# Performance work log

Hardware: AMD Instinct MI355X
Metric: run time of the kernel (lower is better)

The kernel has to match this reference:

```python
import jax, jax.numpy as jnp
import numpy as np

TOP_K = 2
SCALING = 32.0 / 16.0  # alpha / rank


def setup_inputs() -> dict:
    key = jax.random.key(0)
    ks = jax.random.split(key, 8)
    B_, S, D = 4, 4096, 2048
    E, R, H = 5, 16, 256
    return {
        "x": jax.random.normal(ks[0], (B_, S, D), jnp.float32),
        "base_output": jax.random.normal(ks[1], (B_, S, D), jnp.float32),
        "A": jax.random.normal(ks[2], (E, D, R), jnp.float32) * (1.0 / R),
        "B": jax.random.normal(ks[3], (E, R, D), jnp.float32) * 0.02,
        "W1": jax.random.normal(ks[4], (D, H), jnp.float32) * (1.0 / np.sqrt(D)),
        "b1": jnp.zeros((H,), jnp.float32),
        "W2": jax.random.normal(ks[5], (H, E), jnp.float32) * (1.0 / np.sqrt(H)),
        "b2": jnp.zeros((E,), jnp.float32),
    }


def reference(x, base_output, A, B, W1, b1, W2, b2):
    # Router: Linear -> SiLU -> Linear -> softmax
    routing_logits = jax.nn.silu(x @ W1 + b1) @ W2 + b2          # [B,S,E]
    routing_weights = jax.nn.softmax(routing_logits, axis=-1)
    top_k_weights, top_k_indices = jax.lax.top_k(routing_weights, TOP_K)  # [B,S,K]
    top_k_weights = top_k_weights / top_k_weights.sum(-1, keepdims=True)

    # Dense per-expert LoRA eval (faithful to original): x @ A_e @ B_e * scaling
    low = jnp.einsum('bsd,edr->bser', x, A)                       # [B,S,E,R]
    expert_outputs = jnp.einsum('bser,erd->bsed', low, B) * SCALING  # [B,S,E,D]

    # Gather selected experts and combine with normalized weights
    gathered = jnp.take_along_axis(expert_outputs, top_k_indices[..., None], axis=2)  # [B,S,K,D]
    combined = (gathered * top_k_weights[..., None]).sum(axis=2)  # [B,S,D]
    return base_output + combined
```

## Files before the change

kernel.cpp:

```cpp
#include <hip/hip_runtime.h>
#include <math.h>

#define N_TOK 16384
#define D_DIM 2048
#define H_DIM 256
#define E_NUM 5
#define R_DIM 16
#define ER 80

#define NCT 21
#define KG_N 64

typedef _Float16 half8 __attribute__((ext_vector_type(8)));
typedef float f32x4 __attribute__((ext_vector_type(4)));

__global__ __launch_bounds__(256) void pack_w_kernel(
    const float* __restrict__ W1, const float* __restrict__ A,
    _Float16* __restrict__ Whi, _Float16* __restrict__ Wlo) {
  const int idx = blockIdx.x * 256 + threadIdx.x;
  const int lane = idx & 63;
  const int kgct = idx >> 6;
  const int kg = kgct & 63;
  const int ct = kgct >> 6;
  const int k0 = kg * 32 + ((lane >> 4) << 3);
  const int par = lane & 15;
  float v[8];
  if (ct < 16) {
    const int col = ct * 16 + par;
#pragma unroll
    for (int j = 0; j < 8; ++j) v[j] = W1[(size_t)(k0 + j) * H_DIM + col];
  } else {
    const float* Ae = A + (size_t)(ct - 16) * D_DIM * R_DIM;
#pragma unroll
    for (int j = 0; j < 8; ++j) v[j] = Ae[(size_t)(k0 + j) * R_DIM + par];
  }
  half8 hv, lv;
#pragma unroll
  for (int j = 0; j < 8; ++j) {
    const _Float16 hh = (_Float16)v[j];
    hv[j] = hh;
    lv[j] = (_Float16)(v[j] - (float)hh);
  }
  ((half8*)Whi)[(size_t)kgct * 64 + lane] = hv;
  ((half8*)Wlo)[(size_t)kgct * 64 + lane] = lv;
}

__global__ __launch_bounds__(256, 3) void xgemm_kernel(
    const float* __restrict__ x, const float* __restrict__ b1,
    const _Float16* __restrict__ Whi, const _Float16* __restrict__ Wlo,
    float* __restrict__ h, float* __restrict__ P) {
  __shared__ _Float16 lds[2][2][4][64][8];
  const int t = threadIdx.x;
  const int tok0 = blockIdx.x * 64;
  const int y = blockIdx.y;
  const int lane = t & 63;
  const int w = t >> 6;
  const int sr = t >> 2;
  const int sq = t & 3;
  const int lq = lane >> 4;
  const int lp = lane & 15;

  const float* xrow = x + (size_t)(tok0 + sr) * D_DIM + (sq << 3);

  {
    float xv[8];
    *(float4*)&xv[0] = *(const float4*)(xrow);
    *(float4*)&xv[4] = *(const float4*)(xrow + 4);
    half8 hv, lv;
#pragma unroll
    for (int j = 0; j < 8; ++j) {
      const _Float16 hh = (_Float16)xv[j];
      hv[j] = hh;
      lv[j] = (_Float16)(xv[j] - (float)hh);
    }
    *(half8*)&lds[0][0][sq][sr][0] = hv;
    *(half8*)&lds[0][1][sq][sr][0] = lv;
  }

  const half8* WH = (const half8*)Whi;
  const half8* WL = (const half8*)Wlo;

  if (y < 2) {
    f32x4 acc[4][2];
#pragma unroll
    for (int i = 0; i < 4; ++i)
#pragma unroll
      for (int j = 0; j < 2; ++j) acc[i][j] = (f32x4)0.f;
    const int ctg0 = (y << 3) + (w << 1);
    int cur = 0;
    for (int kg = 0; kg < KG_N; ++kg) {
      __syncthreads();
      float xv[8];
      if (kg < KG_N - 1) {
        *(float4*)&xv[0] = *(const float4*)(xrow + (kg + 1) * 32);
        *(float4*)&xv[4] = *(const float4*)(xrow + (kg + 1) * 32 + 4);
      }
      half8 bh[2], bl[2], ah[4], al[4];
#pragma unroll
      for (int ct = 0; ct < 2; ++ct) {
        const size_t wo = ((size_t)(ctg0 + ct) * 64 + kg) * 64 + lane;
        bh[ct] = WH[wo];
        bl[ct] = WL[wo];
      }
#pragma unroll
      for (int rt = 0; rt < 4; ++rt) {
        ah[rt] = *(const half8*)&lds[cur][0][lq][(rt << 4) + lp][0];
        al[rt] = *(const half8*)&lds[cur][1][lq][(rt << 4) + lp][0];
      }
#pragma unroll
      for (int rt = 0; rt < 4; ++rt)
#pragma unroll
        for (int ct = 0; ct < 2; ++ct) {
          acc[rt][ct] = __builtin_amdgcn_mfma_f32_16x16x32_f16(al[rt], bh[ct], acc[rt][ct], 0, 0, 0);
          acc[rt][ct] = __builtin_amdgcn_mfma_f32_16x16x32_f16(ah[rt], bl[ct], acc[rt][ct], 0, 0, 0);
          acc[rt][ct] = __builtin_amdgcn_mfma_f32_16x16x32_f16(ah[rt], bh[ct], acc[rt][ct], 0, 0, 0);
        }
      if (kg < KG_N - 1) {
        half8 hv, lv;
#pragma unroll
        for (int j = 0; j < 8; ++j) {
          const _Float16 hh = (_Float16)xv[j];
          hv[j] = hh;
          lv[j] = (_Float16)(xv[j] - (float)hh);
        }
        *(half8*)&lds[cur ^ 1][0][sq][sr][0] = hv;
        *(half8*)&lds[cur ^ 1][1][sq][sr][0] = lv;
      }
      cur ^= 1;
    }
    const int colb = (y << 7) + (w << 5);
#pragma unroll
    for (int rt = 0; rt < 4; ++rt)
#pragma unroll
      for (int ct = 0; ct < 2; ++ct) {
        const int col = colb + (ct << 4) + lp;
        const float bb = b1[col];
#pragma unroll
        for (int rg = 0; rg < 4; ++rg) {
          const int row = tok0 + (rt << 4) + (lq << 2) + rg;
          float v = acc[rt][ct][rg] + bb;
          v = v / (1.f + expf(-v));
          h[(size_t)row * H_DIM + col] = v;
        }
      }
  } else {
    f32x4 acc[5];
#pragma unroll
    for (int j = 0; j < 5; ++j) acc[j] = (f32x4)0.f;
    int cur = 0;
    for (int kg = 0; kg < KG_N; ++kg) {
      __syncthreads();
      float xv[8];
      if (kg < KG_N - 1) {
        *(float4*)&xv[0] = *(const float4*)(xrow + (kg + 1) * 32);
        *(float4*)&xv[4] = *(const float4*)(xrow + (kg + 1) * 32 + 4);
      }
      half8 bh[5], bl[5];
#pragma unroll
      for (int ct = 0; ct < 5; ++ct) {
        const size_t wo = ((size_t)(16 + ct) * 64 + kg) * 64 + lane;
        bh[ct] = WH[wo];
        bl[ct] = WL[wo];
      }
      const half8 ah = *(const half8*)&lds[cur][0][lq][(w << 4) + lp][0];
      const half8 al = *(const half8*)&lds[cur][1][lq][(w << 4) + lp][0];
#pragma unroll
      for (int ct = 0; ct < 5; ++ct) {
        acc[ct] = __builtin_amdgcn_mfma_f32_16x16x32_f16(al, bh[ct], acc[ct], 0, 0, 0);
        acc[ct] = __builtin_amdgcn_mfma_f32_16x16x32_f16(ah, bl[ct], acc[ct], 0, 0, 0);
        acc[ct] = __builtin_amdgcn_mfma_f32_16x16x32_f16(ah, bh[ct], acc[ct], 0, 0, 0);
      }
      if (kg < KG_N - 1) {
        half8 hv, lv;
#pragma unroll
        for (int j = 0; j < 8; ++j) {
          const _Float16 hh = (_Float16)xv[j];
          hv[j] = hh;
          lv[j] = (_Float16)(xv[j] - (float)hh);
        }
        *(half8*)&lds[cur ^ 1][0][sq][sr][0] = hv;
        *(half8*)&lds[cur ^ 1][1][sq][sr][0] = lv;
      }
      cur ^= 1;
    }
#pragma unroll
    for (int ct = 0; ct < 5; ++ct)
#pragma unroll
      for (int rg = 0; rg < 4; ++rg) {
        const int row = tok0 + (w << 4) + (lq << 2) + rg;
        P[(size_t)row * ER + (ct << 4) + lp] = acc[ct][rg];
      }
  }
}

__global__ __launch_bounds__(256) void route_kernel(
    const float* __restrict__ h, const float* __restrict__ W2,
    const float* __restrict__ b2, float* __restrict__ P) {
  __shared__ float w2s[H_DIM * E_NUM];
  const int t = threadIdx.x;
  for (int i = t; i < H_DIM * E_NUM; i += 256) w2s[i] = W2[i];
  __syncthreads();

  const int tok = blockIdx.x * 64 + (t >> 2);
  const int part = t & 3;
  float p[5] = {0.f, 0.f, 0.f, 0.f, 0.f};
  const float* hr = h + (size_t)tok * H_DIM + part * 64;
#pragma unroll
  for (int i = 0; i < 16; ++i) {
    float hv[4];
    *(float4*)hv = *(const float4*)(hr + (i << 2));
#pragma unroll
    for (int u = 0; u < 4; ++u) {
      const int c = part * 64 + (i << 2) + u;
#pragma unroll
      for (int e = 0; e < 5; ++e) p[e] = fmaf(hv[u], w2s[c * 5 + e], p[e]);
    }
  }
#pragma unroll
  for (int e = 0; e < 5; ++e) {
    p[e] += __shfl_xor(p[e], 1, 64);
    p[e] += __shfl_xor(p[e], 2, 64);
    p[e] += b2[e];
  }
  int e0 = 0;
#pragma unroll
  for (int e = 1; e < 5; ++e) if (p[e] > p[e0]) e0 = e;
  int e1 = (e0 == 0) ? 1 : 0;
#pragma unroll
  for (int e = 0; e < 5; ++e) if (e != e0 && p[e] > p[e1]) e1 = e;
  const float q = expf(p[e1] - p[e0]);
  const float s0 = 2.f / (1.f + q);
  const float s1 = q * s0;

  float* pr = P + (size_t)tok * ER + part * 20;
#pragma unroll
  for (int g = 0; g < 5; ++g) {
    float pv[4];
    *(float4*)pv = *(const float4*)(pr + (g << 2));
#pragma unroll
    for (int u = 0; u < 4; ++u) {
      const int e = (part * 20 + (g << 2) + u) >> 4;
      const float s = (e == e0) ? s0 : ((e == e1) ? s1 : 0.f);
      pv[u] *= s;
    }
    *(float4*)(pr + (g << 2)) = *(float4*)pv;
  }
}

__global__ __launch_bounds__(256) void combine_kernel(
    const float* __restrict__ P, const float* __restrict__ Bm,
    const float* __restrict__ base, float* __restrict__ out) {
  const int t = threadIdx.x;
  const int wg = __builtin_amdgcn_readfirstlane(t >> 6);
  const int c4 = ((blockIdx.x & 7) << 8) + ((t & 63) << 2);
  const int tok0 = ((blockIdx.x >> 3) << 6) + (wg << 4);

  float4 acc[16];
#pragma unroll
  for (int i = 0; i < 16; ++i) acc[i] = make_float4(0.f, 0.f, 0.f, 0.f);

  for (int k0 = 0; k0 < ER; k0 += 4) {
    const float4 bv0 = *(const float4*)(Bm + (size_t)(k0 + 0) * D_DIM + c4);
    const float4 bv1 = *(const float4*)(Bm + (size_t)(k0 + 1) * D_DIM + c4);
    const float4 bv2 = *(const float4*)(Bm + (size_t)(k0 + 2) * D_DIM + c4);
    const float4 bv3 = *(const float4*)(Bm + (size_t)(k0 + 3) * D_DIM + c4);
#pragma unroll
    for (int i = 0; i < 16; ++i) {
      const float* pr = P + (size_t)(tok0 + i) * ER + k0;
      const float p0 = pr[0], p1 = pr[1], p2 = pr[2], p3 = pr[3];
      acc[i].x = fmaf(p0, bv0.x, fmaf(p1, bv1.x, fmaf(p2, bv2.x, fmaf(p3, bv3.x, acc[i].x))));
      acc[i].y = fmaf(p0, bv0.y, fmaf(p1, bv1.y, fmaf(p2, bv2.y, fmaf(p3, bv3.y, acc[i].y))));
      acc[i].z = fmaf(p0, bv0.z, fmaf(p1, bv1.z, fmaf(p2, bv2.z, fmaf(p3, bv3.z, acc[i].z))));
      acc[i].w = fmaf(p0, bv0.w, fmaf(p1, bv1.w, fmaf(p2, bv2.w, fmaf(p3, bv3.w, acc[i].w))));
    }
  }

#pragma unroll
  for (int i = 0; i < 16; ++i) {
    const size_t o = (size_t)(tok0 + i) * D_DIM + c4;
    const float4 b = *(const float4*)(base + o);
    float4 r;
    r.x = acc[i].x + b.x;
    r.y = acc[i].y + b.y;
    r.z = acc[i].z + b.z;
    r.w = acc[i].w + b.w;
    *(float4*)(out + o) = r;
  }
}

extern "C" void kernel_launch(void* const* d_in, const int* in_sizes, int n_in,
                              void* d_out, int out_size, void* d_ws,
                              size_t ws_size, hipStream_t stream) {
  const float* x  = (const float*)d_in[0];
  const float* bo = (const float*)d_in[1];
  const float* A  = (const float*)d_in[2];
  const float* Bm = (const float*)d_in[3];
  const float* W1 = (const float*)d_in[4];
  const float* b1 = (const float*)d_in[5];
  const float* W2 = (const float*)d_in[6];
  const float* b2 = (const float*)d_in[7];
  float* out = (float*)d_out;

  char* ws = (char*)d_ws;
  float* h = (float*)ws;
  float* P = (float*)(ws + 16777216);
  _Float16* Whi = (_Float16*)(ws + 16777216 + 5242880);
  _Float16* Wlo = (_Float16*)(ws + 16777216 + 5242880 + 1376256);

  pack_w_kernel<<<336, 256, 0, stream>>>(W1, A, Whi, Wlo);
  xgemm_kernel<<<dim3(N_TOK / 64, 3), 256, 0, stream>>>(x, b1, Whi, Wlo, h, P);
  route_kernel<<<N_TOK / 64, 256, 0, stream>>>(h, W2, b2, P);
  combine_kernel<<<(N_TOK / 64) * (D_DIM / 256), 256, 0, stream>>>(P, Bm, bo, out);
}
```

Baseline: 459.4 us.

## Fuse router second layer into GEMM epilogue and double K-step with swizzled LDS

The router's SiLU output is no longer written to a hidden buffer. The xgemm epilogue multiplies it by W2 held in shared memory, reduces across lanes with shuffles, and atomically adds partial logits into a buffer that pack_w_kernel zeroes. The route kernel is removed: top-2 selection and the scaling of P now run at the start of combine_kernel, which stages the scaled P tile in LDS. The GEMM main loop also processes 64 K elements per step with an XOR-swizzled LDS layout, halving barriers and aiming to reduce bank conflicts. In exchange it adds atomic traffic, a larger LDS footprint per block, and floating-point summation order that is no longer deterministic.

New measurement: 476.5 us. 3.7% more time.

```diff
diff --git a/kernel.cpp b/kernel.cpp
--- a/kernel.cpp
+++ b/kernel.cpp
@@ -9,15 +9,17 @@
 #define ER 80
 
 #define NCT 21
-#define KG_N 64
+#define KSTEPS 32
 
 typedef _Float16 half8 __attribute__((ext_vector_type(8)));
 typedef float f32x4 __attribute__((ext_vector_type(4)));
 
 __global__ __launch_bounds__(256) void pack_w_kernel(
     const float* __restrict__ W1, const float* __restrict__ A,
-    _Float16* __restrict__ Whi, _Float16* __restrict__ Wlo) {
+    _Float16* __restrict__ Whi, _Float16* __restrict__ Wlo,
+    float* __restrict__ logits) {
   const int idx = blockIdx.x * 256 + threadIdx.x;
+  if (idx < N_TOK * E_NUM) logits[idx] = 0.f;
   const int lane = idx & 63;
   const int kgct = idx >> 6;
   const int kg = kgct & 63;
@@ -48,33 +50,42 @@
 __global__ __launch_bounds__(256, 3) void xgemm_kernel(
     const float* __restrict__ x, const float* __restrict__ b1,
     const _Float16* __restrict__ Whi, const _Float16* __restrict__ Wlo,
-    float* __restrict__ h, float* __restrict__ P) {
-  __shared__ _Float16 lds[2][2][4][64][8];
+    const float* __restrict__ W2, float* __restrict__ logits,
+    float* __restrict__ P) {
+  __shared__ _Float16 lds[2][2][8][64][8];
+  __shared__ float w2s[H_DIM * E_NUM];
   const int t = threadIdx.x;
   const int tok0 = blockIdx.x * 64;
   const int y = blockIdx.y;
   const int lane = t & 63;
   const int w = t >> 6;
   const int sr = t >> 2;
-  const int sq = t & 3;
+  const int q = t & 3;
   const int lq = lane >> 4;
   const int lp = lane & 15;
 
-  const float* xrow = x + (size_t)(tok0 + sr) * D_DIM + (sq << 3);
+  const float* xrow = x + (size_t)(tok0 + sr) * D_DIM + (q << 4);
 
   {
-    float xv[8];
+    float xv[16];
     *(float4*)&xv[0] = *(const float4*)(xrow);
     *(float4*)&xv[4] = *(const float4*)(xrow + 4);
-    half8 hv, lv;
-#pragma unroll
-    for (int j = 0; j < 8; ++j) {
-      const _Float16 hh = (_Float16)xv[j];
-      hv[j] = hh;
-      lv[j] = (_Float16)(xv[j] - (float)hh);
-    }
-    *(half8*)&lds[0][0][sq][sr][0] = hv;
-    *(half8*)&lds[0][1][sq][sr][0] = lv;
+    *(float4*)&xv[8] = *(const float4*)(xrow + 8);
+    *(float4*)&xv[12] = *(const float4*)(xrow + 12);
+#pragma unroll
+    for (int hf = 0; hf < 2; ++hf) {
+      half8 hv, lv;
+#pragma unroll
+      for (int j = 0; j < 8; ++j) {
+        const float v = xv[(hf << 3) + j];
+        const _Float16 hh = (_Float16)v;
+        hv[j] = hh;
+        lv[j] = (_Float16)(v - (float)hh);
+      }
+      const int kq = (q << 1) + hf;
+      *(half8*)&lds[0][0][kq][sr ^ kq][0] = hv;
+      *(half8*)&lds[0][1][kq][sr ^ kq][0] = lv;
+    }
   }
 
   const half8* WH = (const half8*)Whi;
@@ -88,98 +99,153 @@
       for (int j = 0; j < 2; ++j) acc[i][j] = (f32x4)0.f;
     const int ctg0 = (y << 3) + (w << 1);
     int cur = 0;
-    for (int kg = 0; kg < KG_N; ++kg) {
+    for (int kg = 0; kg < KSTEPS; ++kg) {
       __syncthreads();
-      float xv[8];
-      if (kg < KG_N - 1) {
-        *(float4*)&xv[0] = *(const float4*)(xrow + (kg + 1) * 32);
-        *(float4*)&xv[4] = *(const float4*)(xrow + (kg + 1) * 32 + 4);
-      }
-      half8 bh[2], bl[2], ah[4], al[4];
-#pragma unroll
-      for (int ct = 0; ct < 2; ++ct) {
-        const size_t wo = ((size_t)(ctg0 + ct) * 64 + kg) * 64 + lane;
-        bh[ct] = WH[wo];
-        bl[ct] = WL[wo];
-      }
-#pragma unroll
-      for (int rt = 0; rt < 4; ++rt) {
-        ah[rt] = *(const half8*)&lds[cur][0][lq][(rt << 4) + lp][0];
-        al[rt] = *(const half8*)&lds[cur][1][lq][(rt << 4) + lp][0];
-      }
-#pragma unroll
-      for (int rt = 0; rt < 4; ++rt)
-#pragma unroll
-        for (int ct = 0; ct < 2; ++ct) {
-          acc[rt][ct] = __builtin_amdgcn_mfma_f32_16x16x32_f16(al[rt], bh[ct], acc[rt][ct], 0, 0, 0);
-          acc[rt][ct] = __builtin_amdgcn_mfma_f32_16x16x32_f16(ah[rt], bl[ct], acc[rt][ct], 0, 0, 0);
-          acc[rt][ct] = __builtin_amdgcn_mfma_f32_16x16x32_f16(ah[rt], bh[ct], acc[rt][ct], 0, 0, 0);
-        }
-      if (kg < KG_N - 1) {
-        half8 hv, lv;
-#pragma unroll
-        for (int j = 0; j < 8; ++j) {
-          const _Float16 hh = (_Float16)xv[j];
-          hv[j] = hh;
-          lv[j] = (_Float16)(xv[j] - (float)hh);
-        }
-        *(half8*)&lds[cur ^ 1][0][sq][sr][0] = hv;
-        *(half8*)&lds[cur ^ 1][1][sq][sr][0] = lv;
+      float xv[16];
+      const bool more = (kg < KSTEPS - 1);
+      if (more) {
+        const float* src = xrow + (kg + 1) * 64;
+        *(float4*)&xv[0] = *(const float4*)(src);
+        *(float4*)&xv[4] = *(const float4*)(src + 4);
+        *(float4*)&xv[8] = *(const float4*)(src + 8);
+        *(float4*)&xv[12] = *(const float4*)(src + 12);
+      }
+      half8 bh[2][2], bl[2][2];
+#pragma unroll
+      for (int ct = 0; ct < 2; ++ct)
+#pragma unroll
+        for (int h2 = 0; h2 < 2; ++h2) {
+          const size_t wo = ((size_t)(ctg0 + ct) * 64 + (kg << 1) + h2) * 64 + lane;
+          bh[ct][h2] = WH[wo];
+          bl[ct][h2] = WL[wo];
+        }
+#pragma unroll
+      for (int h2 = 0; h2 < 2; ++h2) {
+        const int kq = (h2 << 2) + lq;
+#pragma unroll
+        for (int rt = 0; rt < 4; ++rt) {
+          const int r = ((rt << 4) + lp) ^ kq;
+          const half8 ah = *(const half8*)&lds[cur][0][kq][r][0];
+          const half8 al = *(const half8*)&lds[cur][1][kq][r][0];
+#pragma unroll
+          for (int ct = 0; ct < 2; ++ct) {
+            acc[rt][ct] = __builtin_amdgcn_mfma_f32_16x16x32_f16(al, bh[ct][h2], acc[rt][ct], 0, 0, 0);
+            acc[rt][ct] = __builtin_amdgcn_mfma_f32_16x16x32_f16(ah, bl[ct][h2], acc[rt][ct], 0, 0, 0);
+            acc[rt][ct] = __builtin_amdgcn_mfma_f32_16x16x32_f16(ah, bh[ct][h2], acc[rt][ct], 0, 0, 0);
+          }
+        }
+      }
+      if (more) {
+#pragma unroll
+        for (int hf = 0; hf < 2; ++hf) {
+          half8 hv, lv;
+#pragma unroll
+          for (int j = 0; j < 8; ++j) {
+            const float v = xv[(hf << 3) + j];
+            const _Float16 hh = (_Float16)v;
+            hv[j] = hh;
+            lv[j] = (_Float16)(v - (float)hh);
+          }
+          const int kq = (q << 1) + hf;
+          *(half8*)&lds[cur ^ 1][0][kq][sr ^ kq][0] = hv;
+          *(half8*)&lds[cur ^ 1][1][kq][sr ^ kq][0] = lv;
+        }
       }
       cur ^= 1;
     }
+    for (int i = t; i < H_DIM * E_NUM; i += 256) w2s[i] = W2[i];
+    __syncthreads();
     const int colb = (y << 7) + (w << 5);
 #pragma unroll
-    for (int rt = 0; rt < 4; ++rt)
+    for (int rt = 0; rt < 4; ++rt) {
+      float pl[4][5];
+#pragma unroll
+      for (int rg = 0; rg < 4; ++rg)
+#pragma unroll
+        for (int e = 0; e < 5; ++e) pl[rg][e] = 0.f;
 #pragma unroll
       for (int ct = 0; ct < 2; ++ct) {
         const int col = colb + (ct << 4) + lp;
         const float bb = b1[col];
+        float w2c[5];
+#pragma unroll
+        for (int e = 0; e < 5; ++e) w2c[e] = w2s[col * 5 + e];
 #pragma unroll
         for (int rg = 0; rg < 4; ++rg) {
-          const int row = tok0 + (rt << 4) + (lq << 2) + rg;
           float v = acc[rt][ct][rg] + bb;
           v = v / (1.f + expf(-v));
-          h[(size_t)row * H_DIM + col] = v;
-        }
-      }
+#pragma unroll
+          for (int e = 0; e < 5; ++e) pl[rg][e] = fmaf(v, w2c[e], pl[rg][e]);
+        }
+      }
+#pragma unroll
+      for (int m = 1; m < 16; m <<= 1)
+#pragma unroll
+        for (int rg = 0; rg < 4; ++rg)
+#pragma unroll
+          for (int e = 0; e < 5; ++e) pl[rg][e] += __shfl_xor(pl[rg][e], m, 64);
+      if (lp == 0) {
+        const int row0 = tok0 + (rt << 4) + (lq << 2);
+#pragma unroll
+        for (int rg = 0; rg < 4; ++rg)
+#pragma unroll
+          for (int e = 0; e < 5; ++e)
+            atomicAdd(&logits[(size_t)(row0 + rg) * E_NUM + e], pl[rg][e]);
+      }
+    }
   } else {
     f32x4 acc[5];
 #pragma unroll
     for (int j = 0; j < 5; ++j) acc[j] = (f32x4)0.f;
     int cur = 0;
-    for (int kg = 0; kg < KG_N; ++kg) {
+    for (int kg = 0; kg < KSTEPS; ++kg) {
       __syncthreads();
-      float xv[8];
-      if (kg < KG_N - 1) {
-        *(float4*)&xv[0] = *(const float4*)(xrow + (kg + 1) * 32);
-        *(float4*)&xv[4] = *(const float4*)(xrow + (kg + 1) * 32 + 4);
-      }
-      half8 bh[5], bl[5];
-#pragma unroll
-      for (int ct = 0; ct < 5; ++ct) {
-        const size_t wo = ((size_t)(16 + ct) * 64 + kg) * 64 + lane;
-        bh[ct] = WH[wo];
-        bl[ct] = WL[wo];
-      }
-      const half8 ah = *(const half8*)&lds[cur][0][lq][(w << 4) + lp][0];
-      const half8 al = *(const half8*)&lds[cur][1][lq][(w << 4) + lp][0];
-#pragma unroll
-      for (int ct = 0; ct < 5; ++ct) {
-        acc[ct] = __builtin_amdgcn_mfma_f32_16x16x32_f16(al, bh[ct], acc[ct], 0, 0, 0);
-        acc[ct] = __builtin_amdgcn_mfma_f32_16x16x32_f16(ah, bl[ct], acc[ct], 0, 0, 0);
-        acc[ct] = __builtin_amdgcn_mfma_f32_16x16x32_f16(ah, bh[ct], acc[ct], 0, 0, 0);
-      }
-      if (kg < KG_N - 1) {
-        half8 hv, lv;
-#pragma unroll
-        for (int j = 0; j < 8; ++j) {
-          const _Float16 hh = (_Float16)xv[j];
-          hv[j] = hh;
-          lv[j] = (_Float16)(xv[j] - (float)hh);
-        }
-        *(half8*)&lds[cur ^ 1][0][sq][sr][0] = hv;
-        *(half8*)&lds[cur ^ 1][1][sq][sr][0] = lv;
+      float xv[16];
+      const bool more = (kg < KSTEPS - 1);
+      if (more) {
+        const float* src = xrow + (kg + 1) * 64;
+        *(float4*)&xv[0] = *(const float4*)(src);
+        *(float4*)&xv[4] = *(const float4*)(src + 4);
+        *(float4*)&xv[8] = *(const float4*)(src + 8);
+        *(float4*)&xv[12] = *(const float4*)(src + 12);
+      }
+      half8 bh[5][2], bl[5][2];
+#pragma unroll
+      for (int ct = 0; ct < 5; ++ct)
+#pragma unroll
+        for (int h2 = 0; h2 < 2; ++h2) {
+          const size_t wo = ((size_t)(16 + ct) * 64 + (kg << 1) + h2) * 64 + lane;
+          bh[ct][h2] = WH[wo];
+          bl[ct][h2] = WL[wo];
+        }
+#pragma unroll
+      for (int h2 = 0; h2 < 2; ++h2) {
+        const int kq = (h2 << 2) + lq;
+        const int r = ((w << 4) + lp) ^ kq;
+        const half8 ah = *(const half8*)&lds[cur][0][kq][r][0];
+        const half8 al = *(const half8*)&lds[cur][1][kq][r][0];
+#pragma unroll
+        for (int ct = 0; ct < 5; ++ct) {
+          acc[ct] = __builtin_amdgcn_mfma_f32_16x16x32_f16(al, bh[ct][h2], acc[ct], 0, 0, 0);
+          acc[ct] = __builtin_amdgcn_mfma_f32_16x16x32_f16(ah, bl[ct][h2], acc[ct], 0, 0, 0);
+          acc[ct] = __builtin_amdgcn_mfma_f32_16x16x32_f16(ah, bh[ct][h2], acc[ct], 0, 0, 0);
+        }
+      }
+      if (more) {
+#pragma unroll
+        for (int hf = 0; hf < 2; ++hf) {
+          half8 hv, lv;
+#pragma unroll
+          for (int j = 0; j < 8; ++j) {
+            const float v = xv[(hf << 3) + j];
+            const _Float16 hh = (_Float16)v;
+            hv[j] = hh;
+            lv[j] = (_Float16)(v - (float)hh);
+          }
+          const int kq = (q << 1) + hf;
+          *(half8*)&lds[cur ^ 1][0][kq][sr ^ kq][0] = hv;
+          *(half8*)&lds[cur ^ 1][1][kq][sr ^ kq][0] = lv;
+        }
       }
       cur ^= 1;
     }
@@ -193,71 +259,56 @@
   }
 }
 
-__global__ __launch_bounds__(256) void route_kernel(
-    const float* __restrict__ h, const float* __restrict__ W2,
-    const float* __restrict__ b2, float* __restrict__ P) {
-  __shared__ float w2s[H_DIM * E_NUM];
-  const int t = threadIdx.x;
-  for (int i = t; i < H_DIM * E_NUM; i += 256) w2s[i] = W2[i];
-  __syncthreads();
-
-  const int tok = blockIdx.x * 64 + (t >> 2);
-  const int part = t & 3;
-  float p[5] = {0.f, 0.f, 0.f, 0.f, 0.f};
-  const float* hr = h + (size_t)tok * H_DIM + part * 64;
-#pragma unroll
-  for (int i = 0; i < 16; ++i) {
-    float hv[4];
-    *(float4*)hv = *(const float4*)(hr + (i << 2));
-#pragma unroll
-    for (int u = 0; u < 4; ++u) {
-      const int c = part * 64 + (i << 2) + u;
-#pragma unroll
-      for (int e = 0; e < 5; ++e) p[e] = fmaf(hv[u], w2s[c * 5 + e], p[e]);
-    }
-  }
-#pragma unroll
-  for (int e = 0; e < 5; ++e) {
-    p[e] += __shfl_xor(p[e], 1, 64);
-    p[e] += __shfl_xor(p[e], 2, 64);
-    p[e] += b2[e];
-  }
-  int e0 = 0;
-#pragma unroll
-  for (int e = 1; e < 5; ++e) if (p[e] > p[e0]) e0 = e;
-  int e1 = (e0 == 0) ? 1 : 0;
-#pragma unroll
-  for (int e = 0; e < 5; ++e) if (e != e0 && p[e] > p[e1]) e1 = e;
-  const float q = expf(p[e1] - p[e0]);
-  const float s0 = 2.f / (1.f + q);
-  const float s1 = q * s0;
-
-  float* pr = P + (size_t)tok * ER + part * 20;
-#pragma unroll
-  for (int g = 0; g < 5; ++g) {
-    float pv[4];
-    *(float4*)pv = *(const float4*)(pr + (g << 2));
-#pragma unroll
-    for (int u = 0; u < 4; ++u) {
-      const int e = (part * 20 + (g << 2) + u) >> 4;
-      const float s = (e == e0) ? s0 : ((e == e1) ? s1 : 0.f);
-      pv[u] *= s;
-    }
-    *(float4*)(pr + (g << 2)) = *(float4*)pv;
-  }
-}
-
 __global__ __launch_bounds__(256) void combine_kernel(
     const float* __restrict__ P, const float* __restrict__ Bm,
-    const float* __restrict__ base, float* __restrict__ out) {
+    const float* __restrict__ base, const float* __restrict__ logits,
+    const float* __restrict__ b2, float* __restrict__ out) {
+  __shared__ float Pl[64][80];
+  __shared__ float sc[64][5];
   const int t = threadIdx.x;
   const int wg = __builtin_amdgcn_readfirstlane(t >> 6);
   const int c4 = ((blockIdx.x & 7) << 8) + ((t & 63) << 2);
-  const int tok0 = ((blockIdx.x >> 3) << 6) + (wg << 4);
+  const int tokb = (blockIdx.x >> 3) << 6;
+
+  if (t < 64) {
+    float lg[5];
+#pragma unroll
+    for (int e = 0; e < 5; ++e)
+      lg[e] = logits[(size_t)(tokb + t) * E_NUM + e] + b2[e];
+    int e0 = 0;
+#pragma unroll
+    for (int e = 1; e < 5; ++e) if (lg[e] > lg[e0]) e0 = e;
+    int e1 = (e0 == 0) ? 1 : 0;
+#pragma unroll
+    for (int e = 0; e < 5; ++e) if (e != e0 && lg[e] > lg[e1]) e1 = e;
+    const float qq = expf(lg[e1] - lg[e0]);
+    const float s0 = 2.f / (1.f + qq);
+    const float s1 = qq * s0;
+#pragma unroll
+    for (int e = 0; e < 5; ++e)
+      sc[t][e] = (e == e0) ? s0 : ((e == e1) ? s1 : 0.f);
+  }
+  __syncthreads();
+  {
+    const int row = t >> 2;
+    const int off = (t & 3) * 20;
+    const float* prow = P + (size_t)(tokb + row) * ER + off;
+#pragma unroll
+    for (int j = 0; j < 5; ++j) {
+      float4 v = *(const float4*)(prow + (j << 2));
+      v.x *= sc[row][(off + (j << 2) + 0) >> 4];
+      v.y *= sc[row][(off + (j << 2) + 1) >> 4];
+      v.z *= sc[row][(off + (j << 2) + 2) >> 4];
+      v.w *= sc[row][(off + (j << 2) + 3) >> 4];
+      *(float4*)&Pl[row][off + (j << 2)] = v;
+    }
+  }
+  __syncthreads();
 
   float4 acc[16];
 #pragma unroll
   for (int i = 0; i < 16; ++i) acc[i] = make_float4(0.f, 0.f, 0.f, 0.f);
+  const int r0 = wg << 4;
 
   for (int k0 = 0; k0 < ER; k0 += 4) {
     const float4 bv0 = *(const float4*)(Bm + (size_t)(k0 + 0) * D_DIM + c4);
@@ -266,18 +317,18 @@
     const float4 bv3 = *(const float4*)(Bm + (size_t)(k0 + 3) * D_DIM + c4);
 #pragma unroll
     for (int i = 0; i < 16; ++i) {
-      const float* pr = P + (size_t)(tok0 + i) * ER + k0;
-      const float p0 = pr[0], p1 = pr[1], p2 = pr[2], p3 = pr[3];
-      acc[i].x = fmaf(p0, bv0.x, fmaf(p1, bv1.x, fmaf(p2, bv2.x, fmaf(p3, bv3.x, acc[i].x))));
-      acc[i].y = fmaf(p0, bv0.y, fmaf(p1, bv1.y, fmaf(p2, bv2.y, fmaf(p3, bv3.y, acc[i].y))));
-      acc[i].z = fmaf(p0, bv0.z, fmaf(p1, bv1.z, fmaf(p2, bv2.z, fmaf(p3, bv3.z, acc[i].z))));
-      acc[i].w = fmaf(p0, bv0.w, fmaf(p1, bv1.w, fmaf(p2, bv2.w, fmaf(p3, bv3.w, acc[i].w))));
+      float pv[4];
+      *(float4*)pv = *(const float4*)&Pl[r0 + i][k0];
+      acc[i].x = fmaf(pv[0], bv0.x, fmaf(pv[1], bv1.x, fmaf(pv[2], bv2.x, fmaf(pv[3], bv3.x, acc[i].x))));
+      acc[i].y = fmaf(pv[0], bv0.y, fmaf(pv[1], bv1.y, fmaf(pv[2], bv2.y, fmaf(pv[3], bv3.y, acc[i].y))));
+      acc[i].z = fmaf(pv[0], bv0.z, fmaf(pv[1], bv1.z, fmaf(pv[2], bv2.z, fmaf(pv[3], bv3.z, acc[i].z))));
+      acc[i].w = fmaf(pv[0], bv0.w, fmaf(pv[1], bv1.w, fmaf(pv[2], bv2.w, fmaf(pv[3], bv3.w, acc[i].w))));
     }
   }
 
 #pragma unroll
   for (int i = 0; i < 16; ++i) {
-    const size_t o = (size_t)(tok0 + i) * D_DIM + c4;
+    const size_t o = (size_t)(tokb + r0 + i) * D_DIM + c4;
     const float4 b = *(const float4*)(base + o);
     float4 r;
     r.x = acc[i].x + b.x;
@@ -302,13 +353,14 @@
   float* out = (float*)d_out;
 
   char* ws = (char*)d_ws;
-  float* h = (float*)ws;
-  float* P = (float*)(ws + 16777216);
-  _Float16* Whi = (_Float16*)(ws + 16777216 + 5242880);
-  _Float16* Wlo = (_Float16*)(ws + 16777216 + 5242880 + 1376256);
-
-  pack_w_kernel<<<336, 256, 0, stream>>>(W1, A, Whi, Wlo);
-  xgemm_kernel<<<dim3(N_TOK / 64, 3), 256, 0, stream>>>(x, b1, Whi, Wlo, h, P);
-  route_kernel<<<N_TOK / 64, 256, 0, stream>>>(h, W2, b2, P);
-  combine_kernel<<<(N_TOK / 64) * (D_DIM / 256), 256, 0, stream>>>(P, Bm, bo, out);
+  float* P = (float*)ws;
+  _Float16* Whi = (_Float16*)(ws + 5242880);
+  _Float16* Wlo = (_Float16*)(ws + 5242880 + 1376256);
+  float* logits = (float*)(ws + 5242880 + 2 * 1376256);
+
+  pack_w_kernel<<<336, 256, 0, stream>>>(W1, A, Whi, Wlo, logits);
+  xgemm_kernel<<<dim3(N_TOK / 64, 3), 256, 0, stream>>>(x, b1, Whi, Wlo, W2,
+                                                        logits, P);
+  combine_kernel<<<(N_TOK / 64) * (D_DIM / 256), 256, 0, stream>>>(
+      P, Bm, bo, logits, b2, out);
 }
```

## Fuse router second layer into GEMM epilogue and routing into combine kernel

Applied to the files above, without the earlier changes.

The SiLU hidden activations are no longer written to global memory. Each router GEMM block now multiplies them by W2 in its epilogue and writes per-half partial logits, and the separate route kernel is removed: top-2 selection and scaling of P happen in the combine kernel, which stages scaled P in LDS with 32-token tiles and double-buffered B loads. The x tile in LDS is also XOR-swizzled to reduce bank conflicts. This removes the 16 MB h round trip and one launch, at the cost of extra shuffles and LDS in the GEMM epilogue and more combine blocks.

Result: faster. 442.0 us (-3.8%).

```diff
diff --git a/kernel.cpp b/kernel.cpp
--- a/kernel.cpp
+++ b/kernel.cpp
@@ -48,8 +48,11 @@
 __global__ __launch_bounds__(256, 3) void xgemm_kernel(
     const float* __restrict__ x, const float* __restrict__ b1,
     const _Float16* __restrict__ Whi, const _Float16* __restrict__ Wlo,
-    float* __restrict__ h, float* __restrict__ P) {
+    const float* __restrict__ W2, float* __restrict__ plog,
+    float* __restrict__ P) {
   __shared__ _Float16 lds[2][2][4][64][8];
+  __shared__ float w2s[H_DIM * E_NUM];
+  __shared__ float plbuf[4][64][E_NUM];
   const int t = threadIdx.x;
   const int tok0 = blockIdx.x * 64;
   const int y = blockIdx.y;
@@ -73,8 +76,8 @@
       hv[j] = hh;
       lv[j] = (_Float16)(xv[j] - (float)hh);
     }
-    *(half8*)&lds[0][0][sq][sr][0] = hv;
-    *(half8*)&lds[0][1][sq][sr][0] = lv;
+    *(half8*)&lds[0][0][sq][sr ^ sq][0] = hv;
+    *(half8*)&lds[0][1][sq][sr ^ sq][0] = lv;
   }
 
   const half8* WH = (const half8*)Whi;
@@ -90,12 +93,14 @@
     int cur = 0;
     for (int kg = 0; kg < KG_N; ++kg) {
       __syncthreads();
+      const bool more = (kg < KG_N - 1);
       float xv[8];
-      if (kg < KG_N - 1) {
-        *(float4*)&xv[0] = *(const float4*)(xrow + (kg + 1) * 32);
-        *(float4*)&xv[4] = *(const float4*)(xrow + (kg + 1) * 32 + 4);
-      }
-      half8 bh[2], bl[2], ah[4], al[4];
+      if (more) {
+        const float* src = xrow + (kg + 1) * 32;
+        *(float4*)&xv[0] = *(const float4*)(src);
+        *(float4*)&xv[4] = *(const float4*)(src + 4);
+      }
+      half8 bh[2], bl[2];
 #pragma unroll
       for (int ct = 0; ct < 2; ++ct) {
         const size_t wo = ((size_t)(ctg0 + ct) * 64 + kg) * 64 + lane;
@@ -104,18 +109,17 @@
       }
 #pragma unroll
       for (int rt = 0; rt < 4; ++rt) {
-        ah[rt] = *(const half8*)&lds[cur][0][lq][(rt << 4) + lp][0];
-        al[rt] = *(const half8*)&lds[cur][1][lq][(rt << 4) + lp][0];
-      }
-#pragma unroll
-      for (int rt = 0; rt < 4; ++rt)
+        const int r = ((rt << 4) + lp) ^ lq;
+        const half8 ah = *(const half8*)&lds[cur][0][lq][r][0];
+        const half8 al = *(const half8*)&lds[cur][1][lq][r][0];
 #pragma unroll
         for (int ct = 0; ct < 2; ++ct) {
-          acc[rt][ct] = __builtin_amdgcn_mfma_f32_16x16x32_f16(al[rt], bh[ct], acc[rt][ct], 0, 0, 0);
-          acc[rt][ct] = __builtin_amdgcn_mfma_f32_16x16x32_f16(ah[rt], bl[ct], acc[rt][ct], 0, 0, 0);
-          acc[rt][ct] = __builtin_amdgcn_mfma_f32_16x16x32_f16(ah[rt], bh[ct], acc[rt][ct], 0, 0, 0);
-        }
-      if (kg < KG_N - 1) {
+          acc[rt][ct] = __builtin_amdgcn_mfma_f32_16x16x32_f16(al, bh[ct], acc[rt][ct], 0, 0, 0);
+          acc[rt][ct] = __builtin_amdgcn_mfma_f32_16x16x32_f16(ah, bl[ct], acc[rt][ct], 0, 0, 0);
+          acc[rt][ct] = __builtin_amdgcn_mfma_f32_16x16x32_f16(ah, bh[ct], acc[rt][ct], 0, 0, 0);
+        }
+      }
+      if (more) {
         half8 hv, lv;
 #pragma unroll
         for (int j = 0; j < 8; ++j) {
@@ -123,26 +127,59 @@
           hv[j] = hh;
           lv[j] = (_Float16)(xv[j] - (float)hh);
         }
-        *(half8*)&lds[cur ^ 1][0][sq][sr][0] = hv;
-        *(half8*)&lds[cur ^ 1][1][sq][sr][0] = lv;
+        *(half8*)&lds[cur ^ 1][0][sq][sr ^ sq][0] = hv;
+        *(half8*)&lds[cur ^ 1][1][sq][sr ^ sq][0] = lv;
       }
       cur ^= 1;
     }
+
+    for (int i = t; i < H_DIM * E_NUM; i += 256) w2s[i] = W2[i];
+    __syncthreads();
     const int colb = (y << 7) + (w << 5);
 #pragma unroll
-    for (int rt = 0; rt < 4; ++rt)
+    for (int rt = 0; rt < 4; ++rt) {
+      float pl[4][5];
+#pragma unroll
+      for (int rg = 0; rg < 4; ++rg)
+#pragma unroll
+        for (int e = 0; e < 5; ++e) pl[rg][e] = 0.f;
 #pragma unroll
       for (int ct = 0; ct < 2; ++ct) {
         const int col = colb + (ct << 4) + lp;
         const float bb = b1[col];
+        float w2c[5];
+#pragma unroll
+        for (int e = 0; e < 5; ++e) w2c[e] = w2s[col * 5 + e];
 #pragma unroll
         for (int rg = 0; rg < 4; ++rg) {
-          const int row = tok0 + (rt << 4) + (lq << 2) + rg;
           float v = acc[rt][ct][rg] + bb;
           v = v / (1.f + expf(-v));
-          h[(size_t)row * H_DIM + col] = v;
-        }
-      }
+#pragma unroll
+          for (int e = 0; e < 5; ++e) pl[rg][e] = fmaf(v, w2c[e], pl[rg][e]);
+        }
+      }
+#pragma unroll
+      for (int m = 1; m < 16; m <<= 1)
+#pragma unroll
+        for (int rg = 0; rg < 4; ++rg)
+#pragma unroll
+          for (int e = 0; e < 5; ++e) pl[rg][e] += __shfl_xor(pl[rg][e], m, 64);
+      if (lp == 0) {
+        const int rl0 = (rt << 4) + (lq << 2);
+#pragma unroll
+        for (int rg = 0; rg < 4; ++rg)
+#pragma unroll
+          for (int e = 0; e < 5; ++e) plbuf[w][rl0 + rg][e] = pl[rg][e];
+      }
+    }
+    __syncthreads();
+    for (int i = t; i < 64 * E_NUM; i += 256) {
+      const int row = i / E_NUM;
+      const int e = i - row * E_NUM;
+      const float s = plbuf[0][row][e] + plbuf[1][row][e] +
+                      plbuf[2][row][e] + plbuf[3][row][e];
+      plog[((size_t)y * N_TOK + tok0 + row) * E_NUM + e] = s;
+    }
   } else {
     f32x4 acc[5];
 #pragma unroll
@@ -150,10 +187,12 @@
     int cur = 0;
     for (int kg = 0; kg < KG_N; ++kg) {
       __syncthreads();
+      const bool more = (kg < KG_N - 1);
       float xv[8];
-      if (kg < KG_N - 1) {
-        *(float4*)&xv[0] = *(const float4*)(xrow + (kg + 1) * 32);
-        *(float4*)&xv[4] = *(const float4*)(xrow + (kg + 1) * 32 + 4);
+      if (more) {
+        const float* src = xrow + (kg + 1) * 32;
+        *(float4*)&xv[0] = *(const float4*)(src);
+        *(float4*)&xv[4] = *(const float4*)(src + 4);
       }
       half8 bh[5], bl[5];
 #pragma unroll
@@ -162,15 +201,18 @@
         bh[ct] = WH[wo];
         bl[ct] = WL[wo];
       }
-      const half8 ah = *(const half8*)&lds[cur][0][lq][(w << 4) + lp][0];
-      const half8 al = *(const half8*)&lds[cur][1][lq][(w << 4) + lp][0];
-#pragma unroll
-      for (int ct = 0; ct < 5; ++ct) {
-        acc[ct] = __builtin_amdgcn_mfma_f32_16x16x32_f16(al, bh[ct], acc[ct], 0, 0, 0);
-        acc[ct] = __builtin_amdgcn_mfma_f32_16x16x32_f16(ah, bl[ct], acc[ct], 0, 0, 0);
-        acc[ct] = __builtin_amdgcn_mfma_f32_16x16x32_f16(ah, bh[ct], acc[ct], 0, 0, 0);
-      }
-      if (kg < KG_N - 1) {
+      {
+        const int r = ((w << 4) + lp) ^ lq;
+        const half8 ah = *(const half8*)&lds[cur][0][lq][r][0];
+        const half8 al = *(const half8*)&lds[cur][1][lq][r][0];
+#pragma unroll
+        for (int ct = 0; ct < 5; ++ct) {
+          acc[ct] = __builtin_amdgcn_mfma_f32_16x16x32_f16(al, bh[ct], acc[ct], 0, 0, 0);
+          acc[ct] = __builtin_amdgcn_mfma_f32_16x16x32_f16(ah, bl[ct], acc[ct], 0, 0, 0);
+          acc[ct] = __builtin_amdgcn_mfma_f32_16x16x32_f16(ah, bh[ct], acc[ct], 0, 0, 0);
+        }
+      }
+      if (more) {
         half8 hv, lv;
 #pragma unroll
         for (int j = 0; j < 8; ++j) {
@@ -178,8 +220,8 @@
           hv[j] = hh;
           lv[j] = (_Float16)(xv[j] - (float)hh);
         }
-        *(half8*)&lds[cur ^ 1][0][sq][sr][0] = hv;
-        *(half8*)&lds[cur ^ 1][1][sq][sr][0] = lv;
+        *(half8*)&lds[cur ^ 1][0][sq][sr ^ sq][0] = hv;
+        *(half8*)&lds[cur ^ 1][1][sq][sr ^ sq][0] = lv;
       }
       cur ^= 1;
     }
@@ -193,91 +235,91 @@
   }
 }
 
-__global__ __launch_bounds__(256) void route_kernel(
-    const float* __restrict__ h, const float* __restrict__ W2,
-    const float* __restrict__ b2, float* __restrict__ P) {
-  __shared__ float w2s[H_DIM * E_NUM];
-  const int t = threadIdx.x;
-  for (int i = t; i < H_DIM * E_NUM; i += 256) w2s[i] = W2[i];
-  __syncthreads();
-
-  const int tok = blockIdx.x * 64 + (t >> 2);
-  const int part = t & 3;
-  float p[5] = {0.f, 0.f, 0.f, 0.f, 0.f};
-  const float* hr = h + (size_t)tok * H_DIM + part * 64;
-#pragma unroll
-  for (int i = 0; i < 16; ++i) {
-    float hv[4];
-    *(float4*)hv = *(const float4*)(hr + (i << 2));
-#pragma unroll
-    for (int u = 0; u < 4; ++u) {
-      const int c = part * 64 + (i << 2) + u;
-#pragma unroll
-      for (int e = 0; e < 5; ++e) p[e] = fmaf(hv[u], w2s[c * 5 + e], p[e]);
-    }
-  }
-#pragma unroll
-  for (int e = 0; e < 5; ++e) {
-    p[e] += __shfl_xor(p[e], 1, 64);
-    p[e] += __shfl_xor(p[e], 2, 64);
-    p[e] += b2[e];
-  }
-  int e0 = 0;
-#pragma unroll
-  for (int e = 1; e < 5; ++e) if (p[e] > p[e0]) e0 = e;
-  int e1 = (e0 == 0) ? 1 : 0;
-#pragma unroll
-  for (int e = 0; e < 5; ++e) if (e != e0 && p[e] > p[e1]) e1 = e;
-  const float q = expf(p[e1] - p[e0]);
-  const float s0 = 2.f / (1.f + q);
-  const float s1 = q * s0;
-
-  float* pr = P + (size_t)tok * ER + part * 20;
-#pragma unroll
-  for (int g = 0; g < 5; ++g) {
-    float pv[4];
-    *(float4*)pv = *(const float4*)(pr + (g << 2));
-#pragma unroll
-    for (int u = 0; u < 4; ++u) {
-      const int e = (part * 20 + (g << 2) + u) >> 4;
-      const float s = (e == e0) ? s0 : ((e == e1) ? s1 : 0.f);
-      pv[u] *= s;
-    }
-    *(float4*)(pr + (g << 2)) = *(float4*)pv;
-  }
-}
-
-__global__ __launch_bounds__(256) void combine_kernel(
+__global__ __launch_bounds__(256, 4) void combine_kernel(
     const float* __restrict__ P, const float* __restrict__ Bm,
-    const float* __restrict__ base, float* __restrict__ out) {
+    const float* __restrict__ base, const float* __restrict__ plog,
+    const float* __restrict__ b2, float* __restrict__ out) {
+  __shared__ float Pl[32][80];
+  __shared__ float sc[32][5];
   const int t = threadIdx.x;
   const int wg = __builtin_amdgcn_readfirstlane(t >> 6);
   const int c4 = ((blockIdx.x & 7) << 8) + ((t & 63) << 2);
-  const int tok0 = ((blockIdx.x >> 3) << 6) + (wg << 4);
-
-  float4 acc[16];
-#pragma unroll
-  for (int i = 0; i < 16; ++i) acc[i] = make_float4(0.f, 0.f, 0.f, 0.f);
-
-  for (int k0 = 0; k0 < ER; k0 += 4) {
-    const float4 bv0 = *(const float4*)(Bm + (size_t)(k0 + 0) * D_DIM + c4);
-    const float4 bv1 = *(const float4*)(Bm + (size_t)(k0 + 1) * D_DIM + c4);
-    const float4 bv2 = *(const float4*)(Bm + (size_t)(k0 + 2) * D_DIM + c4);
-    const float4 bv3 = *(const float4*)(Bm + (size_t)(k0 + 3) * D_DIM + c4);
-#pragma unroll
-    for (int i = 0; i < 16; ++i) {
-      const float* pr = P + (size_t)(tok0 + i) * ER + k0;
-      const float p0 = pr[0], p1 = pr[1], p2 = pr[2], p3 = pr[3];
-      acc[i].x = fmaf(p0, bv0.x, fmaf(p1, bv1.x, fmaf(p2, bv2.x, fmaf(p3, bv3.x, acc[i].x))));
-      acc[i].y = fmaf(p0, bv0.y, fmaf(p1, bv1.y, fmaf(p2, bv2.y, fmaf(p3, bv3.y, acc[i].y))));
-      acc[i].z = fmaf(p0, bv0.z, fmaf(p1, bv1.z, fmaf(p2, bv2.z, fmaf(p3, bv3.z, acc[i].z))));
-      acc[i].w = fmaf(p0, bv0.w, fmaf(p1, bv1.w, fmaf(p2, bv2.w, fmaf(p3, bv3.w, acc[i].w))));
-    }
-  }
-
-#pragma unroll
-  for (int i = 0; i < 16; ++i) {
-    const size_t o = (size_t)(tok0 + i) * D_DIM + c4;
+  const int tokb = (blockIdx.x >> 3) << 5;
+  const int r0 = wg << 3;
+
+  if (t < 32) {
+    const float* p0 = plog + (size_t)(tokb + t) * E_NUM;
+    const float* p1 = plog + ((size_t)N_TOK + tokb + t) * E_NUM;
+    float lg[5];
+#pragma unroll
+    for (int e = 0; e < 5; ++e) lg[e] = p0[e] + p1[e] + b2[e];
+    int e0 = 0;
+#pragma unroll
+    for (int e = 1; e < 5; ++e) if (lg[e] > lg[e0]) e0 = e;
+    int e1 = (e0 == 0) ? 1 : 0;
+#pragma unroll
+    for (int e = 0; e < 5; ++e) if (e != e0 && lg[e] > lg[e1]) e1 = e;
+    const float qq = expf(lg[e1] - lg[e0]);
+    const float s0 = 2.f / (1.f + qq);
+    const float s1 = qq * s0;
+#pragma unroll
+    for (int e = 0; e < 5; ++e)
+      sc[t][e] = (e == e0) ? s0 : ((e == e1) ? s1 : 0.f);
+  }
+  __syncthreads();
+  for (int idx = t; idx < 640; idx += 256) {
+    const int row = idx / 20;
+    const int off = (idx % 20) << 2;
+    float4 v = *(const float4*)(P + (size_t)(tokb + row) * ER + off);
+    v.x *= sc[row][(off + 0) >> 4];
+    v.y *= sc[row][(off + 1) >> 4];
+    v.z *= sc[row][(off + 2) >> 4];
+    v.w *= sc[row][(off + 3) >> 4];
+    *(float4*)&Pl[row][off] = v;
+  }
+  __syncthreads();
+
+  float4 acc[8];
+#pragma unroll
+  for (int i = 0; i < 8; ++i) acc[i] = make_float4(0.f, 0.f, 0.f, 0.f);
+
+  float4 bmA[4], bmB[4];
+#pragma unroll
+  for (int r = 0; r < 4; ++r)
+    bmA[r] = *(const float4*)(Bm + (size_t)r * D_DIM + c4);
+
+  for (int k0 = 0; k0 < ER; k0 += 8) {
+#pragma unroll
+    for (int r = 0; r < 4; ++r)
+      bmB[r] = *(const float4*)(Bm + (size_t)(k0 + 4 + r) * D_DIM + c4);
+#pragma unroll
+    for (int i = 0; i < 8; ++i) {
+      float pv[4];
+      *(float4*)pv = *(const float4*)&Pl[r0 + i][k0];
+      acc[i].x = fmaf(pv[0], bmA[0].x, fmaf(pv[1], bmA[1].x, fmaf(pv[2], bmA[2].x, fmaf(pv[3], bmA[3].x, acc[i].x))));
+      acc[i].y = fmaf(pv[0], bmA[0].y, fmaf(pv[1], bmA[1].y, fmaf(pv[2], bmA[2].y, fmaf(pv[3], bmA[3].y, acc[i].y))));
+      acc[i].z = fmaf(pv[0], bmA[0].z, fmaf(pv[1], bmA[1].z, fmaf(pv[2], bmA[2].z, fmaf(pv[3], bmA[3].z, acc[i].z))));
+      acc[i].w = fmaf(pv[0], bmA[0].w, fmaf(pv[1], bmA[1].w, fmaf(pv[2], bmA[2].w, fmaf(pv[3], bmA[3].w, acc[i].w))));
+    }
+    if (k0 + 8 < ER) {
+#pragma unroll
+      for (int r = 0; r < 4; ++r)
+        bmA[r] = *(const float4*)(Bm + (size_t)(k0 + 8 + r) * D_DIM + c4);
+    }
+#pragma unroll
+    for (int i = 0; i < 8; ++i) {
+      float pv[4];
+      *(float4*)pv = *(const float4*)&Pl[r0 + i][k0 + 4];
+      acc[i].x = fmaf(pv[0], bmB[0].x, fmaf(pv[1], bmB[1].x, fmaf(pv[2], bmB[2].x, fmaf(pv[3], bmB[3].x, acc[i].x))));
+      acc[i].y = fmaf(pv[0], bmB[0].y, fmaf(pv[1], bmB[1].y, fmaf(pv[2], bmB[2].y, fmaf(pv[3], bmB[3].y, acc[i].y))));
+      acc[i].z = fmaf(pv[0], bmB[0].z, fmaf(pv[1], bmB[1].z, fmaf(pv[2], bmB[2].z, fmaf(pv[3], bmB[3].z, acc[i].z))));
+      acc[i].w = fmaf(pv[0], bmB[0].w, fmaf(pv[1], bmB[1].w, fmaf(pv[2], bmB[2].w, fmaf(pv[3], bmB[3].w, acc[i].w))));
+    }
+  }
+
+#pragma unroll
+  for (int i = 0; i < 8; ++i) {
+    const size_t o = (size_t)(tokb + r0 + i) * D_DIM + c4;
     const float4 b = *(const float4*)(base + o);
     float4 r;
     r.x = acc[i].x + b.x;
@@ -302,13 +344,14 @@
   float* out = (float*)d_out;
 
   char* ws = (char*)d_ws;
-  float* h = (float*)ws;
-  float* P = (float*)(ws + 16777216);
-  _Float16* Whi = (_Float16*)(ws + 16777216 + 5242880);
-  _Float16* Wlo = (_Float16*)(ws + 16777216 + 5242880 + 1376256);
+  float* P = (float*)ws;
+  _Float16* Whi = (_Float16*)(ws + 5242880);
+  _Float16* Wlo = (_Float16*)(ws + 5242880 + 1376256);
+  float* plog = (float*)(ws + 5242880 + 2 * 1376256);
 
   pack_w_kernel<<<336, 256, 0, stream>>>(W1, A, Whi, Wlo);
-  xgemm_kernel<<<dim3(N_TOK / 64, 3), 256, 0, stream>>>(x, b1, Whi, Wlo, h, P);
-  route_kernel<<<N_TOK / 64, 256, 0, stream>>>(h, W2, b2, P);
-  combine_kernel<<<(N_TOK / 64) * (D_DIM / 256), 256, 0, stream>>>(P, Bm, bo, out);
+  xgemm_kernel<<<dim3(N_TOK / 64, 3), 256, 0, stream>>>(x, b1, Whi, Wlo, W2,
+                                                        plog, P);
+  combine_kernel<<<(N_TOK / 32) * (D_DIM / 256), 256, 0, stream>>>(
+      P, Bm, bo, plog, b2, out);
 }
```
